# Optimization experiments

Measured on AMD Instinct MI355X. Metric: run time of the kernel, lower is better.

Reference implementation:

```python
import jax, jax.numpy as jnp
import numpy as np

NUM_EMBEDDINGS = 1024
DIM = 256
COMMIT = 0.25


def setup_inputs() -> dict:
    key = jax.random.key(0)
    k_inp, k_emb = jax.random.split(key)
    inp = jax.random.normal(k_inp, (64, 1024, DIM), dtype=jnp.float32)
    # emb.weight.data.uniform_(-1/num_embeddings, 1/num_embeddings)
    emb = jax.random.uniform(
        k_emb, (NUM_EMBEDDINGS, DIM), dtype=jnp.float32,
        minval=-1.0 / NUM_EMBEDDINGS, maxval=1.0 / NUM_EMBEDDINGS)
    return {"inp": inp, "emb": emb}


def reference(inp, emb):
    flat = inp.reshape(-1, DIM)                       # [N, D]
    d = (jnp.sum(flat * flat, axis=1, keepdims=True)
         + jnp.sum(emb * emb, axis=1)
         - 2.0 * flat @ emb.T)
    idx = jnp.argmin(d, axis=1)                       # [N]
    # gather instead of one-hot matmul (same math)
    quant = emb[idx].reshape(inp.shape)               # [B, T, D]
    codebook_loss = jnp.mean((jax.lax.stop_gradient(quant) - inp) ** 2)
    commit_loss = jnp.mean((quant - jax.lax.stop_gradient(inp)) ** 2)
    loss = codebook_loss + COMMIT * commit_loss
    st = inp + jax.lax.stop_gradient(quant - inp)     # straight-through
    return st, loss, idx
```

## Files before the change

### kernel.cpp

```cpp
#include <hip/hip_runtime.h>
#include <math.h>

#define D 256
#define K 1024
#define NR 65536
#define ST_SIZE (NR * D)
#define LOSS_OFF ST_SIZE
#define IDX_OFF (ST_SIZE + 1)
#define BM 128
#define TPB 512
#define NRND 32
#define NBLK (NR / BM)
#define MARGIN 2e-3f
#define CAND_CAP 3072

typedef short bf16x8 __attribute__((ext_vector_type(8)));
typedef float f32x4 __attribute__((ext_vector_type(4)));

#define GLDS(g, s) __builtin_amdgcn_global_load_lds( \
    (const __attribute__((address_space(1))) unsigned int*)(g), \
    (__attribute__((address_space(3))) unsigned int*)(s), 16, 0, 0)

__device__ __forceinline__ unsigned f2bf(float f) {
    unsigned u = __float_as_uint(f);
    return (u + 0x7FFFu + ((u >> 16) & 1u)) >> 16;
}
__device__ __forceinline__ uint4 packB(float4 a, float4 b) {
    uint4 w;
    w.x = f2bf(-2.f * a.x) | (f2bf(-2.f * a.y) << 16);
    w.y = f2bf(-2.f * a.z) | (f2bf(-2.f * a.w) << 16);
    w.z = f2bf(-2.f * b.x) | (f2bf(-2.f * b.y) << 16);
    w.w = f2bf(-2.f * b.z) | (f2bf(-2.f * b.w) << 16);
    return w;
}

__device__ __forceinline__ float sq_nf(float x) {
    float s = x * x;
    asm volatile("" : "+v"(s));
    return s;
}
template <typename F>
__device__ __forceinline__ float np_sumsq256(F ld) {
    float tot[2];
    #pragma unroll
    for (int h = 0; h < 2; ++h) {
        const int base = h * 128;
        float r[8];
        #pragma unroll
        for (int j = 0; j < 8; ++j) r[j] = sq_nf(ld(base + j));
        for (int i = 8; i < 128; i += 8) {
            #pragma unroll
            for (int j = 0; j < 8; ++j) r[j] += sq_nf(ld(base + i + j));
        }
        tot[h] = ((r[0] + r[1]) + (r[2] + r[3])) + ((r[4] + r[5]) + (r[6] + r[7]));
    }
    return tot[0] + tot[1];
}

__global__ void prep_kernel(const float* __restrict__ emb,
                            unsigned short* __restrict__ pb,
                            float* __restrict__ se) {
    if (blockIdx.x < 128) {
        const int c  = blockIdx.x * 256 + threadIdx.x;
        const int ct = c >> 9;
        const int r  = c & 511;
        const int kb = r >> 6, l = r & 63;
        const float* srcp = emb + (size_t)(ct * 16 + (l & 15)) * D
                                + kb * 32 + (l >> 4) * 8;
        const float4* s4 = (const float4*)srcp;
        ((uint4*)pb)[c] = packB(s4[0], s4[1]);
    } else {
        const int k = (blockIdx.x - 128) * 256 + threadIdx.x;
        const float* row = emb + (size_t)k * D;
        se[k] = np_sumsq256([&](int i) { return row[i]; });
    }
}

__global__ __attribute__((amdgpu_waves_per_eu(2, 4))) __launch_bounds__(TPB)
void vq_main(const float* __restrict__ inp, const float* __restrict__ emb,
             const unsigned short* __restrict__ pb, const float* __restrict__ se,
             float* __restrict__ out, double* __restrict__ lsum) {
    __shared__ __align__(16) unsigned short Bt[3][8192];
    __shared__ float sx_s[BM];
    __shared__ float rfin[BM];
    __shared__ unsigned cand[CAND_CAP];
    __shared__ float candsc[CAND_CAP];
    __shared__ unsigned bestd[BM];
    __shared__ unsigned bestc[BM];
    __shared__ int ncand;

    const int t   = threadIdx.x;
    const int ws  = t >> 6;
    const int l   = t & 63;
    const int c16 = l & 15;
    const int g4  = l >> 4;
    const int r0  = blockIdx.x * BM;

    if (t < BM) { bestd[t] = 0xFFFFFFFFu; bestc[t] = 0xFFFFFFFFu; }
    if (t == 0) ncand = 0;

    bf16x8 afr[8];
    {
        const float* xrow = inp + (size_t)(r0 + ws * 16 + c16) * D;
        #pragma unroll
        for (int kb = 0; kb < 8; ++kb) {
            const float4* p4 = (const float4*)(xrow + kb * 32 + g4 * 8);
            float4 a = p4[0], b = p4[1];
            bf16x8 v;
            v[0] = (short)f2bf(a.x); v[1] = (short)f2bf(a.y);
            v[2] = (short)f2bf(a.z); v[3] = (short)f2bf(a.w);
            v[4] = (short)f2bf(b.x); v[5] = (short)f2bf(b.y);
            v[6] = (short)f2bf(b.z); v[7] = (short)f2bf(b.w);
            afr[kb] = v;
        }
    }

    {
        const int slot = t & 15, grp = t >> 4;
        const int j = slot & 7, h = slot >> 3;
        #pragma unroll
        for (int p = 0; p < 4; ++p) {
            const int row = p * 32 + grp;
            const float* base = inp + (size_t)(r0 + row) * D + h * 128 + j;
            float s = sq_nf(base[0]);
            #pragma unroll
            for (int i = 1; i < 16; ++i) s += sq_nf(base[i * 8]);
            #pragma unroll
            for (int m = 1; m <= 8; m <<= 1) s += __shfl_xor(s, m);
            if (slot == 0) sx_s[row] = s;
        }
    }

    float rmin[4];
    #pragma unroll
    for (int i = 0; i < 4; ++i) rmin[i] = INFINITY;

    const uint4* srcv = (const uint4*)pb;

    auto stage = [&](int buf, int cr) {
        const uint4* g = srcv + (size_t)cr * 1024;
        #pragma unroll
        for (int q = 0; q < 2; ++q) {
            char* lbase = (char*)&Bt[buf][0] + (q * 512 + ws * 64) * 16;
            GLDS(g + q * TPB + t, lbase);
        }
    };

    stage(0, 0);
    stage(1, 1);
    for (int cr = 0; cr < NRND; ++cr) {
        asm volatile("s_waitcnt vmcnt(2) lgkmcnt(0)" ::: "memory");
        __builtin_amdgcn_s_barrier();
        __builtin_amdgcn_sched_barrier(0);
        if (cr + 2 < NRND) stage((cr + 2) % 3, cr + 2);
        const bf16x8* bch = (const bf16x8*)&Bt[cr % 3][0];
        f32x4 a0e, a0o, a1e, a1o;
        {
            const float sev0 = se[(cr * 2 + 0) * 16 + c16];
            const float sev1 = se[(cr * 2 + 1) * 16 + c16];
            #pragma unroll
            for (int i = 0; i < 4; ++i) { a0e[i] = sev0; a0o[i] = 0.f; a1e[i] = sev1; a1o[i] = 0.f; }
        }
        #pragma unroll
        for (int kb = 0; kb < 8; kb += 2) {
            a0e = __builtin_amdgcn_mfma_f32_16x16x32_bf16(afr[kb],     bch[kb * 64 + l],             a0e, 0, 0, 0);
            a1e = __builtin_amdgcn_mfma_f32_16x16x32_bf16(afr[kb],     bch[512 + kb * 64 + l],       a1e, 0, 0, 0);
            a0o = __builtin_amdgcn_mfma_f32_16x16x32_bf16(afr[kb + 1], bch[(kb + 1) * 64 + l],       a0o, 0, 0, 0);
            a1o = __builtin_amdgcn_mfma_f32_16x16x32_bf16(afr[kb + 1], bch[512 + (kb + 1) * 64 + l], a1o, 0, 0, 0);
        }
        float sc0[4], sc1[4];
        #pragma unroll
        for (int i = 0; i < 4; ++i) { sc0[i] = a0e[i] + a0o[i]; sc1[i] = a1e[i] + a1o[i]; }

        #pragma unroll
        for (int i = 0; i < 4; ++i) rmin[i] = fminf(rmin[i], fminf(sc0[i], sc1[i]));
        if ((cr & 1) == 0) {
            #pragma unroll
            for (int i = 0; i < 4; ++i) {
                #pragma unroll
                for (int m = 1; m <= 8; m <<= 1)
                    rmin[i] = fminf(rmin[i], __shfl_xor(rmin[i], m));
            }
        }
        #pragma unroll
        for (int i = 0; i < 4; ++i) {
            const int row_local = ws * 16 + g4 * 4 + i;
            if (sc0[i] <= rmin[i] + MARGIN) {
                const int p = atomicAdd(&ncand, 1);
                if (p < CAND_CAP) {
                    cand[p]   = ((unsigned)row_local << 10) | (unsigned)((cr * 2) * 16 + c16);
                    candsc[p] = sc0[i];
                }
            }
            if (sc1[i] <= rmin[i] + MARGIN) {
                const int p = atomicAdd(&ncand, 1);
                if (p < CAND_CAP) {
                    cand[p]   = ((unsigned)row_local << 10) | (unsigned)((cr * 2 + 1) * 16 + c16);
                    candsc[p] = sc1[i];
                }
            }
        }
    }
    #pragma unroll
    for (int i = 0; i < 4; ++i) {
        #pragma unroll
        for (int m = 1; m <= 8; m <<= 1)
            rmin[i] = fminf(rmin[i], __shfl_xor(rmin[i], m));
    }
    if (c16 == 0) {
        #pragma unroll
        for (int i = 0; i < 4; ++i)
            rfin[ws * 16 + g4 * 4 + i] = rmin[i];
    }
    __syncthreads();

    int n = ncand; if (n > CAND_CAP) n = CAND_CAP;
    {
        const int qw = l >> 4, lq = l & 15;
        for (int ci = ws * 4 + qw; ci < n; ci += 32) {
            const unsigned uc = cand[ci];
            const int row_local = uc >> 10, code = uc & 1023;
            const float sc = candsc[ci];
            if (sc <= rfin[row_local] + MARGIN) {
                const float4* xp = (const float4*)(inp + (size_t)(r0 + row_local) * D) + lq * 4;
                const float4* ep = (const float4*)(emb + (size_t)code * D) + lq * 4;
                float p = 0.f;
                #pragma unroll
                for (int q = 0; q < 4; ++q) {
                    float4 x = xp[q], e = ep[q];
                    p = fmaf(x.x, e.x, p);
                    p = fmaf(x.y, e.y, p);
                    p = fmaf(x.z, e.z, p);
                    p = fmaf(x.w, e.w, p);
                }
                #pragma unroll
                for (int m = 1; m <= 8; m <<= 1) p += __shfl_xor(p, m);
                const float tv = sx_s[row_local] + se[code];
                const float d  = fmaf(-2.f, p, tv);
                if (lq == 0) {
                    candsc[ci] = d;
                    atomicMin(&bestd[row_local], __float_as_uint(d));
                }
            } else if (lq == 0) {
                candsc[ci] = INFINITY;
            }
        }
    }
    __syncthreads();
    for (int ci = t; ci < n; ci += TPB) {
        const unsigned uc = cand[ci];
        if (__float_as_uint(candsc[ci]) == bestd[uc >> 10])
            atomicMin(&bestc[uc >> 10], uc & 1023u);
    }
    __syncthreads();
    if (t < BM) out[IDX_OFF + r0 + t] = (float)bestc[t];

    {
        float4* out4 = (float4*)(out + (size_t)r0 * D);
        const float4* emb4 = (const float4*)emb;
        #pragma unroll
        for (int i = 0; i < (BM * D) / (4 * TPB); ++i) {
            const int e = i * TPB + t;
            out4[e] = emb4[((size_t)bestc[e >> 6] << 6) + (e & 63)];
        }
    }

    if (t < 64) {
        double s = (double)__uint_as_float(bestd[t]) + (double)__uint_as_float(bestd[t + 64]);
        #pragma unroll
        for (int m = 1; m < 64; m <<= 1) s += __shfl_xor(s, m);
        if (t == 0) lsum[blockIdx.x] = s;
    }
}

__global__ void fin_kernel(const double* __restrict__ lsum, float* __restrict__ out) {
    const int l = threadIdx.x;
    double s = 0.0;
    #pragma unroll
    for (int i = 0; i < NBLK / 64; ++i) s += lsum[l * (NBLK / 64) + i];
    #pragma unroll
    for (int m = 1; m < 64; m <<= 1) s += __shfl_xor(s, m);
    if (l == 0) out[LOSS_OFF] = (float)(1.25 * s / (double)ST_SIZE);
}

extern "C" void kernel_launch(void* const* d_in, const int* in_sizes, int n_in,
                              void* d_out, int out_size, void* d_ws, size_t ws_size,
                              hipStream_t stream) {
    const float* inp = (const float*)d_in[0];
    const float* emb = (const float*)d_in[1];
    float* out = (float*)d_out;
    unsigned short* pb = (unsigned short*)d_ws;
    float*  se_ws      = (float*)((char*)d_ws + 524288);
    double* lsum       = (double*)((char*)d_ws + 528384);

    prep_kernel<<<132, 256, 0, stream>>>(emb, pb, se_ws);
    vq_main<<<NBLK, TPB, 0, stream>>>(inp, emb, pb, se_ws, out, lsum);
    fin_kernel<<<1, 64, 0, stream>>>(lsum, out);
}
```

Measured before the change: 142.4 us.

## Fuse loss finalize via atomics, cache codebook norms in LDS, interleave row norms

Drops the separate finalize kernel. Each block now atomically adds its loss partial into a global double, and the last block to finish, found through an atomic done counter, writes the final loss; a memset zeroes the accumulators before launch. Codebook squared norms are copied into shared memory once per block instead of being read from global memory in every round. The per-row input squared-norm computation is moved into the first four pipeline rounds so it overlaps with the staged loads. The trade-offs are a memset launch in place of the finalize launch, an extra 4 KB of LDS per block, and double atomics that make the loss summation order nondeterministic.

```diff
diff --git a/kernel.cpp b/kernel.cpp
--- a/kernel.cpp
+++ b/kernel.cpp
@@ -79,8 +79,10 @@
 __global__ __attribute__((amdgpu_waves_per_eu(2, 4))) __launch_bounds__(TPB)
 void vq_main(const float* __restrict__ inp, const float* __restrict__ emb,
              const unsigned short* __restrict__ pb, const float* __restrict__ se,
-             float* __restrict__ out, double* __restrict__ lsum) {
+             float* __restrict__ out, double* __restrict__ loss_acc,
+             unsigned* __restrict__ done_ctr) {
     __shared__ __align__(16) unsigned short Bt[3][8192];
+    __shared__ float se_s[K];
     __shared__ float sx_s[BM];
     __shared__ float rfin[BM];
     __shared__ unsigned cand[CAND_CAP];
@@ -98,6 +100,8 @@
 
     if (t < BM) { bestd[t] = 0xFFFFFFFFu; bestc[t] = 0xFFFFFFFFu; }
     if (t == 0) ncand = 0;
+    #pragma unroll
+    for (int i = 0; i < K / TPB; ++i) se_s[i * TPB + t] = se[i * TPB + t];
 
     bf16x8 afr[8];
     {
@@ -115,22 +119,6 @@
         }
     }
 
-    {
-        const int slot = t & 15, grp = t >> 4;
-        const int j = slot & 7, h = slot >> 3;
-        #pragma unroll
-        for (int p = 0; p < 4; ++p) {
-            const int row = p * 32 + grp;
-            const float* base = inp + (size_t)(r0 + row) * D + h * 128 + j;
-            float s = sq_nf(base[0]);
-            #pragma unroll
-            for (int i = 1; i < 16; ++i) s += sq_nf(base[i * 8]);
-            #pragma unroll
-            for (int m = 1; m <= 8; m <<= 1) s += __shfl_xor(s, m);
-            if (slot == 0) sx_s[row] = s;
-        }
-    }
-
     float rmin[4];
     #pragma unroll
     for (int i = 0; i < 4; ++i) rmin[i] = INFINITY;
@@ -152,12 +140,24 @@
         asm volatile("s_waitcnt vmcnt(2) lgkmcnt(0)" ::: "memory");
         __builtin_amdgcn_s_barrier();
         __builtin_amdgcn_sched_barrier(0);
+        if (cr < 4) {
+            const int slot = t & 15, grp = t >> 4;
+            const int j = slot & 7, h = slot >> 3;
+            const int row = cr * 32 + grp;
+            const float* base = inp + (size_t)(r0 + row) * D + h * 128 + j;
+            float s = sq_nf(base[0]);
+            #pragma unroll
+            for (int i = 1; i < 16; ++i) s += sq_nf(base[i * 8]);
+            #pragma unroll
+            for (int m = 1; m <= 8; m <<= 1) s += __shfl_xor(s, m);
+            if (slot == 0) sx_s[row] = s;
+        }
         if (cr + 2 < NRND) stage((cr + 2) % 3, cr + 2);
         const bf16x8* bch = (const bf16x8*)&Bt[cr % 3][0];
         f32x4 a0e, a0o, a1e, a1o;
         {
-            const float sev0 = se[(cr * 2 + 0) * 16 + c16];
-            const float sev1 = se[(cr * 2 + 1) * 16 + c16];
+            const float sev0 = se_s[(cr * 2 + 0) * 16 + c16];
+            const float sev1 = se_s[(cr * 2 + 1) * 16 + c16];
             #pragma unroll
             for (int i = 0; i < 4; ++i) { a0e[i] = sev0; a0o[i] = 0.f; a1e[i] = sev1; a1o[i] = 0.f; }
         }
@@ -235,7 +235,7 @@
                 }
                 #pragma unroll
                 for (int m = 1; m <= 8; m <<= 1) p += __shfl_xor(p, m);
-                const float tv = sx_s[row_local] + se[code];
+                const float tv = sx_s[row_local] + se_s[code];
                 const float d  = fmaf(-2.f, p, tv);
                 if (lq == 0) {
                     candsc[ci] = d;
@@ -269,18 +269,16 @@
         double s = (double)__uint_as_float(bestd[t]) + (double)__uint_as_float(bestd[t + 64]);
         #pragma unroll
         for (int m = 1; m < 64; m <<= 1) s += __shfl_xor(s, m);
-        if (t == 0) lsum[blockIdx.x] = s;
-    }
-}
-
-__global__ void fin_kernel(const double* __restrict__ lsum, float* __restrict__ out) {
-    const int l = threadIdx.x;
-    double s = 0.0;
-    #pragma unroll
-    for (int i = 0; i < NBLK / 64; ++i) s += lsum[l * (NBLK / 64) + i];
-    #pragma unroll
-    for (int m = 1; m < 64; m <<= 1) s += __shfl_xor(s, m);
-    if (l == 0) out[LOSS_OFF] = (float)(1.25 * s / (double)ST_SIZE);
+        if (t == 0) {
+            atomicAdd(loss_acc, s);
+            __threadfence();
+            const unsigned old = atomicAdd(done_ctr, 1u);
+            if (old == (unsigned)(NBLK - 1)) {
+                const double tot = atomicAdd(loss_acc, 0.0);
+                out[LOSS_OFF] = (float)(1.25 * tot / (double)ST_SIZE);
+            }
+        }
+    }
 }
 
 extern "C" void kernel_launch(void* const* d_in, const int* in_sizes, int n_in,
@@ -291,9 +289,10 @@
     float* out = (float*)d_out;
     unsigned short* pb = (unsigned short*)d_ws;
     float*  se_ws      = (float*)((char*)d_ws + 524288);
-    double* lsum       = (double*)((char*)d_ws + 528384);
-
+    double* loss_acc   = (double*)((char*)d_ws + 528384);
+    unsigned* done_ctr = (unsigned*)((char*)d_ws + 528392);
+
+    hipMemsetAsync((char*)d_ws + 528384, 0, 16, stream);
     prep_kernel<<<132, 256, 0, stream>>>(emb, pb, se_ws);
-    vq_main<<<NBLK, TPB, 0, stream>>>(inp, emb, pb, se_ws, out, lsum);
-    fin_kernel<<<1, 64, 0, stream>>>(lsum, out);
-}
+    vq_main<<<NBLK, TPB, 0, stream>>>(inp, emb, pb, se_ws, out, loss_acc, done_ctr);
+}
```

Measured after the change: 154.7 us. +8.6%, slower.
